# Kernel tuning notes

Measured on AMD Instinct MI355X. Metric: run time of the kernel, lower is better.

## Reference

```python
import jax, jax.numpy as jnp
import numpy as np

BATCH, N_CONCEPTS, EMBED_DIM = 16384, 4096, 64
CURVATURE = 1.0
EPS = 1e-7
BALL_SCALE = 0.05  # keep points inside the Poincare ball (c*||x||^2 < 1)


def setup_inputs() -> dict:
    key = jax.random.key(0)
    k1, k2 = jax.random.split(key)
    embeddings = BALL_SCALE * jax.random.normal(k1, (BATCH, EMBED_DIM), dtype=jnp.float32)
    prototypes = BALL_SCALE * jax.random.normal(k2, (N_CONCEPTS, EMBED_DIM), dtype=jnp.float32)
    return {"embeddings": embeddings, "prototypes": prototypes}


def poincare_pairwise(x, p, c):
    # x: (B, D) points, p: (N, D) prototypes -> (B, N) hyperbolic distances.
    # d(x,y) = (1/sqrt(c)) * acosh(1 + 2c*||x-y||^2 / ((1 - c||x||^2)(1 - c||y||^2)))
    x2 = jnp.sum(x * x, axis=-1)                     # (B,)
    p2 = jnp.sum(p * p, axis=-1)                     # (N,)
    xp = x @ p.T                                     # (B, N) single fused GEMM
    sq = jnp.maximum(x2[:, None] + p2[None, :] - 2.0 * xp, 0.0)  # (B, N)
    denom = jnp.maximum((1.0 - c * x2)[:, None] * (1.0 - c * p2)[None, :], EPS)
    arg = 1.0 + 2.0 * c * sq / denom
    return jnp.arccosh(jnp.maximum(arg, 1.0 + EPS)) / jnp.sqrt(c)


def reference(embeddings, prototypes) -> jnp.ndarray:
    # Vectorized equivalent of the per-concept Python loop over prototypes.
    return poincare_pairwise(embeddings, prototypes, CURVATURE)  # (B, N)
```

## Files before the change

kernel.cpp:

```cpp
#include <hip/hip_runtime.h>
#include <hip/hip_bf16.h>


constexpr int BATCH = 16384;
constexpr int NCON  = 4096;
constexpr int DIM   = 64;
constexpr int TM    = 128;
constexpr int TN    = 128;
constexpr int NT_N  = NCON / TN;
constexpr float EPS = 1e-7f;

typedef float  f32x4  __attribute__((ext_vector_type(4)));
typedef __bf16 bf16x8 __attribute__((ext_vector_type(8)));

__global__ __launch_bounds__(256, 2)
void poincare_pairwise_kernel(const float* __restrict__ emb,
                              const float* __restrict__ proto,
                              float* __restrict__ out)
{
    __shared__ __bf16 As[TM * DIM];
    __shared__ __bf16 Bs[TN * DIM];
    __shared__ float  x2s[TM];
    __shared__ float  p2s[TN];

    const int tid = threadIdx.x;
    const int bid = blockIdx.x;
    const int mt  = bid >> 5;
    const int nt  = bid & (NT_N - 1);
    const int m0  = mt * TM;
    const int n0  = nt * TN;

    #pragma unroll
    for (int p = 0; p < 8; ++p) {
        int flat = p * 256 + tid;
        int row  = flat >> 4;
        int kq   = flat & 15;
        f32x4 v = *reinterpret_cast<const f32x4*>(emb + (size_t)(m0 + row) * DIM + kq * 4);
        float ss = v.x * v.x + v.y * v.y + v.z * v.z + v.w * v.w;
        ss += __shfl_xor(ss, 1);
        ss += __shfl_xor(ss, 2);
        ss += __shfl_xor(ss, 4);
        ss += __shfl_xor(ss, 8);
        if (kq == 0) x2s[row] = ss;
        __bf16 b4[4] = {(__bf16)v.x, (__bf16)v.y, (__bf16)v.z, (__bf16)v.w};
        int ke = (kq * 4) ^ ((row & 7) << 3);
        *reinterpret_cast<uint2*>(&As[row * DIM + ke]) = *reinterpret_cast<const uint2*>(b4);
    }
    #pragma unroll
    for (int p = 0; p < 8; ++p) {
        int flat = p * 256 + tid;
        int row  = flat >> 4;
        int kq   = flat & 15;
        f32x4 v = *reinterpret_cast<const f32x4*>(proto + (size_t)(n0 + row) * DIM + kq * 4);
        float ss = v.x * v.x + v.y * v.y + v.z * v.z + v.w * v.w;
        ss += __shfl_xor(ss, 1);
        ss += __shfl_xor(ss, 2);
        ss += __shfl_xor(ss, 4);
        ss += __shfl_xor(ss, 8);
        if (kq == 0) p2s[row] = ss;
        __bf16 b4[4] = {(__bf16)v.x, (__bf16)v.y, (__bf16)v.z, (__bf16)v.w};
        int ke = (kq * 4) ^ ((row & 7) << 3);
        *reinterpret_cast<uint2*>(&Bs[row * DIM + ke]) = *reinterpret_cast<const uint2*>(b4);
    }
    __syncthreads();

    const int lane = tid & 63;
    const int wid  = tid >> 6;
    const int wr   = wid >> 1;
    const int wc   = wid & 1;
    const int lr   = lane & 15;
    const int lk   = (lane >> 4) * 8;

    bf16x8 af[4][2], bfr[4][2];
    #pragma unroll
    for (int m = 0; m < 4; ++m) {
        int row = wr * 64 + m * 16 + lr;
        #pragma unroll
        for (int kk = 0; kk < 2; ++kk) {
            int ke = (kk * 32 + lk) ^ ((row & 7) << 3);
            af[m][kk] = *reinterpret_cast<const bf16x8*>(&As[row * DIM + ke]);
        }
    }
    #pragma unroll
    for (int n = 0; n < 4; ++n) {
        int row = wc * 64 + n * 16 + lr;
        #pragma unroll
        for (int kk = 0; kk < 2; ++kk) {
            int ke = (kk * 32 + lk) ^ ((row & 7) << 3);
            bfr[n][kk] = *reinterpret_cast<const bf16x8*>(&Bs[row * DIM + ke]);
        }
    }

    f32x4 acc[4][4] = {};
    #pragma unroll
    for (int kk = 0; kk < 2; ++kk)
        #pragma unroll
        for (int m = 0; m < 4; ++m)
            #pragma unroll
            for (int n = 0; n < 4; ++n)
                acc[m][n] = __builtin_amdgcn_mfma_f32_16x16x32_bf16(
                    af[m][kk], bfr[n][kk], acc[m][n], 0, 0, 0);

    const int rq = (lane >> 4) * 4;
    #pragma unroll
    for (int m = 0; m < 4; ++m) {
        int rloc0 = wr * 64 + m * 16 + rq;
        #pragma unroll
        for (int n = 0; n < 4; ++n) {
            int cloc = wc * 64 + n * 16 + lr;
            float p2 = p2s[cloc];
            size_t cg = (size_t)(n0 + cloc);
            #pragma unroll
            for (int j = 0; j < 4; ++j) {
                int   rloc = rloc0 + j;
                float x2   = x2s[rloc];
                float xp   = acc[m][n][j];
                float sq   = fmaxf(x2 + p2 - 2.0f * xp, 0.0f);
                float den  = fmaxf((1.0f - x2) * (1.0f - p2), EPS);
                float t    = 2.0f * sq * __builtin_amdgcn_rcpf(den);
                t = fmaxf(t, EPS);
                float s = __builtin_amdgcn_sqrtf(t * (t + 2.0f));
                float d = 0.693147180559945f * __builtin_amdgcn_logf(1.0f + t + s);
                out[(size_t)(m0 + rloc) * NCON + cg] = d;
            }
        }
    }
}

extern "C" void kernel_launch(void* const* d_in, const int* in_sizes, int n_in,
                              void* d_out, int out_size, void* d_ws, size_t ws_size,
                              hipStream_t stream) {
    const float* emb   = (const float*)d_in[0];
    const float* proto = (const float*)d_in[1];
    float* out = (float*)d_out;

    dim3 grid((BATCH / TM) * (NCON / TN));
    dim3 block(256);
    poincare_pairwise_kernel<<<grid, block, 0, stream>>>(emb, proto, out);
}
```

Measured before the change: 74.36 us.

## Swap MFMA operands for row-contiguous float4 nontemporal output stores

Puts prototypes in the MFMA A slot and embeddings in the B slot, so each lane's four accumulator values map to four consecutive output columns of one row. This allows 16-byte vectorized nontemporal stores in place of scalar strided stores. It also interleaves the LDS fragment loads per k-step to reduce live registers, raises launch bounds to 4 blocks per SM, and drops the EPS clamps on the denominator and t. Dropping the clamps assumes inputs stay strictly inside the ball. Without the t clamp, values where rounding makes t negative could give NaN or a small value below the reference's floor.

New measurement: 82.69 us. 11.2% more time.

```diff
diff --git a/kernel.cpp b/kernel.cpp
--- a/kernel.cpp
+++ b/kernel.cpp
@@ -8,12 +8,12 @@
 constexpr int TM    = 128;
 constexpr int TN    = 128;
 constexpr int NT_N  = NCON / TN;
-constexpr float EPS = 1e-7f;
+constexpr float LN2 = 0.6931471805599453f;
 
 typedef float  f32x4  __attribute__((ext_vector_type(4)));
 typedef __bf16 bf16x8 __attribute__((ext_vector_type(8)));
 
-__global__ __launch_bounds__(256, 2)
+__global__ __launch_bounds__(256, 4)
 void poincare_pairwise_kernel(const float* __restrict__ emb,
                               const float* __restrict__ proto,
                               float* __restrict__ out)
@@ -66,63 +66,54 @@
 
     const int lane = tid & 63;
     const int wid  = tid >> 6;
-    const int wr   = wid >> 1;
-    const int wc   = wid & 1;
+    const int wp   = wid >> 1;
+    const int wx   = wid & 1;
     const int lr   = lane & 15;
     const int lk   = (lane >> 4) * 8;
 
-    bf16x8 af[4][2], bfr[4][2];
+    f32x4 acc[4][4] = {};
     #pragma unroll
-    for (int m = 0; m < 4; ++m) {
-        int row = wr * 64 + m * 16 + lr;
+    for (int kk = 0; kk < 2; ++kk) {
+        bf16x8 pfrag[4], xfrag[4];
         #pragma unroll
-        for (int kk = 0; kk < 2; ++kk) {
-            int ke = (kk * 32 + lk) ^ ((row & 7) << 3);
-            af[m][kk] = *reinterpret_cast<const bf16x8*>(&As[row * DIM + ke]);
+        for (int i = 0; i < 4; ++i) {
+            int prow = wp * 64 + i * 16 + lr;
+            int kep  = (kk * 32 + lk) ^ ((prow & 7) << 3);
+            pfrag[i] = *reinterpret_cast<const bf16x8*>(&Bs[prow * DIM + kep]);
+            int xrow = wx * 64 + i * 16 + lr;
+            int kex  = (kk * 32 + lk) ^ ((xrow & 7) << 3);
+            xfrag[i] = *reinterpret_cast<const bf16x8*>(&As[xrow * DIM + kex]);
         }
-    }
-    #pragma unroll
-    for (int n = 0; n < 4; ++n) {
-        int row = wc * 64 + n * 16 + lr;
         #pragma unroll
-        for (int kk = 0; kk < 2; ++kk) {
-            int ke = (kk * 32 + lk) ^ ((row & 7) << 3);
-            bfr[n][kk] = *reinterpret_cast<const bf16x8*>(&Bs[row * DIM + ke]);
-        }
+        for (int i = 0; i < 4; ++i)
+            #pragma unroll
+            for (int n = 0; n < 4; ++n)
+                acc[i][n] = __builtin_amdgcn_mfma_f32_16x16x32_bf16(
+                    pfrag[i], xfrag[n], acc[i][n], 0, 0, 0);
     }
 
-    f32x4 acc[4][4] = {};
+    const int g4 = (lane >> 4) * 4;
     #pragma unroll
-    for (int kk = 0; kk < 2; ++kk)
+    for (int xf = 0; xf < 4; ++xf) {
+        int   xloc = wx * 64 + xf * 16 + lr;
+        float x2   = x2s[xloc];
+        float omx  = 1.0f - x2;
+        float* rowp = out + (size_t)(m0 + xloc) * NCON + n0;
         #pragma unroll
-        for (int m = 0; m < 4; ++m)
-            #pragma unroll
-            for (int n = 0; n < 4; ++n)
-                acc[m][n] = __builtin_amdgcn_mfma_f32_16x16x32_bf16(
-                    af[m][kk], bfr[n][kk], acc[m][n], 0, 0, 0);
-
-    const int rq = (lane >> 4) * 4;
-    #pragma unroll
-    for (int m = 0; m < 4; ++m) {
-        int rloc0 = wr * 64 + m * 16 + rq;
-        #pragma unroll
-        for (int n = 0; n < 4; ++n) {
-            int cloc = wc * 64 + n * 16 + lr;
-            float p2 = p2s[cloc];
-            size_t cg = (size_t)(n0 + cloc);
+        for (int pf = 0; pf < 4; ++pf) {
+            int   ploc = wp * 64 + pf * 16 + g4;
+            f32x4 p2   = *reinterpret_cast<const f32x4*>(&p2s[ploc]);
+            f32x4 dv;
             #pragma unroll
             for (int j = 0; j < 4; ++j) {
-                int   rloc = rloc0 + j;
-                float x2   = x2s[rloc];
-                float xp   = acc[m][n][j];
-                float sq   = fmaxf(x2 + p2 - 2.0f * xp, 0.0f);
-                float den  = fmaxf((1.0f - x2) * (1.0f - p2), EPS);
-                float t    = 2.0f * sq * __builtin_amdgcn_rcpf(den);
-                t = fmaxf(t, EPS);
-                float s = __builtin_amdgcn_sqrtf(t * (t + 2.0f));
-                float d = 0.693147180559945f * __builtin_amdgcn_logf(1.0f + t + s);
-                out[(size_t)(m0 + rloc) * NCON + cg] = d;
+                float xp  = acc[pf][xf][j];
+                float sq  = fmaxf(x2 + p2[j] - 2.0f * xp, 0.0f);
+                float den = omx * (1.0f - p2[j]);
+                float t   = 2.0f * sq * __builtin_amdgcn_rcpf(den);
+                float s   = __builtin_amdgcn_sqrtf(t * (t + 2.0f));
+                dv[j]     = LN2 * __builtin_amdgcn_logf(1.0f + t + s);
             }
+            __builtin_nontemporal_store(dv, reinterpret_cast<f32x4*>(rowp + ploc));
         }
     }
 }
```
